# Kernel optimization log

Hardware: AMD Instinct MI355X
Metric: run time of the kernel (lower is better)

Reference implementation:

```python
import jax, jax.numpy as jnp
import numpy as np

B = 1048576
CARDS = np.array([2,2,2,2,2,3,3,4,4,4,4,4,4,5,5,5,5,5,5,5,2,2,2,2,2,2,2,2,2], dtype=np.int32)
NBR = 29  # number of categorical branches
EPS = 1e-5


def setup_inputs() -> dict:
    key = jax.random.key(0)
    ks = jax.random.split(key, 24)
    inp = {}
    inp['xcon'] = jax.random.normal(ks[0], (B, 7), dtype=jnp.float32)
    raw = jax.random.randint(ks[1], (B, NBR), 0, 5, dtype=jnp.int32)
    inp['xcat'] = raw % jnp.asarray(CARDS)[None, :]  # in-range per-branch indices
    s6 = 1.0 / np.sqrt(6.0)
    inp['emb_tables'] = jax.random.normal(ks[2], (NBR, 5, 6), dtype=jnp.float32)
    inp['w1'] = jax.random.normal(ks[3], (NBR, 6, 6), dtype=jnp.float32) * s6
    inp['b1'] = jax.random.normal(ks[4], (NBR, 6), dtype=jnp.float32) * s6
    inp['w2'] = jax.random.normal(ks[5], (NBR, 6), dtype=jnp.float32) * s6
    inp['b2'] = jax.random.normal(ks[6], (NBR,), dtype=jnp.float32) * s6
    inp['cbn_g'] = jnp.ones((7,), jnp.float32)
    inp['cbn_b'] = jnp.zeros((7,), jnp.float32)
    inp['cbn_m'] = jax.random.normal(ks[7], (7,), jnp.float32) * 0.1
    inp['cbn_v'] = jnp.ones((7,), jnp.float32) + 0.1 * jax.random.uniform(ks[8], (7,))
    dims = [(36, 36), (18, 36), (9, 18), (2, 9)]
    for i, (o, ic) in enumerate(dims, 1):
        s = 1.0 / np.sqrt(ic)
        inp[f'fc{i}_w'] = jax.random.normal(ks[8 + 2 * i], (o, ic), jnp.float32) * s
        inp[f'fc{i}_b'] = jax.random.normal(ks[9 + 2 * i], (o,), jnp.float32) * s
    for i, d in zip([1, 2, 3], [36, 18, 9]):
        inp[f'bn{i}_g'] = jnp.ones((d,), jnp.float32)
        inp[f'bn{i}_b'] = jnp.zeros((d,), jnp.float32)
        inp[f'bn{i}_m'] = jax.random.normal(jax.random.fold_in(key, 100 + i), (d,), jnp.float32) * 0.1
        inp[f'bn{i}_v'] = jnp.ones((d,), jnp.float32) + 0.1 * jax.random.uniform(jax.random.fold_in(key, 200 + i), (d,))
    return inp


def _bn(x, g, b, m, v):
    return (x - m) * jax.lax.rsqrt(v + EPS) * g + b


def reference(xcon, xcat, emb_tables, w1, b1, w2, b2,
              cbn_g, cbn_b, cbn_m, cbn_v,
              fc1_w, fc1_b, bn1_g, bn1_b, bn1_m, bn1_v,
              fc2_w, fc2_b, bn2_g, bn2_b, bn2_m, bn2_v,
              fc3_w, fc3_b, bn3_g, bn3_b, bn3_m, bn3_v,
              fc4_w, fc4_b):
    # Batched gather over all 29 branches: [B,29,6]
    emb = emb_tables[jnp.arange(NBR)[None, :], xcat]
    # Per-branch tiny MLP, fused as batched GEMMs
    h = jax.nn.relu(jnp.einsum('bjd,jde->bje', emb, w1) + b1)   # [B,29,6]
    xcatemb = jnp.einsum('bjd,jd->bj', h, w2) + b2              # [B,29]
    # (catdo_layer dropout is identity in eval mode)
    xcon_n = _bn(xcon, cbn_g, cbn_b, cbn_m, cbn_v)              # BatchNorm1d(7), eval
    xin = jnp.concatenate([xcon_n, xcatemb], axis=1)            # [B,36]
    h1 = jax.nn.relu(_bn(xin @ fc1_w.T + fc1_b, bn1_g, bn1_b, bn1_m, bn1_v))
    h2 = jax.nn.relu(_bn(h1 @ fc2_w.T + fc2_b, bn2_g, bn2_b, bn2_m, bn2_v))
    h3 = jax.nn.relu(_bn(h2 @ fc3_w.T + fc3_b, bn3_g, bn3_b, bn3_m, bn3_v))
    logits = h3 @ fc4_w.T + fc4_b                               # [B,2]
    return jax.nn.softmax(logits, axis=1)
```

## Files before the change

kernel.cpp:

```cpp
#include <hip/hip_runtime.h>

typedef _Float16 f16x8 __attribute__((ext_vector_type(8)));
typedef __fp16 fp16x2 __attribute__((ext_vector_type(2)));
typedef float f32x4 __attribute__((ext_vector_type(4)));

#define NTHR 256
constexpr float EPS = 1e-5f;
constexpr int NBLOCKS = 4096;

#define TAB_B   0
#define W1_B    1024
#define W2_B    7168
#define W3_B    11264
#define B1_B    12288
#define B2_B    12544
#define B3_B    12672
#define W4_B    12736
#define B4_B    12800

__device__ __forceinline__ ushort f16bits(float x) {
    union { _Float16 h; ushort u; } c; c.h = (_Float16)x; return c.u;
}
__device__ __forceinline__ uint pk2(float a, float b) {
    union { fp16x2 h; uint u; } c; c.h = __builtin_amdgcn_cvt_pkrtz(a, b); return c.u;
}
__device__ __forceinline__ uint pkrelu(float a, float b) {
    return pk2(fmaxf(a, 0.f), fmaxf(b, 0.f));
}
__device__ __forceinline__ f16x8 mk8(uint a, uint b, uint c, uint d) {
    union { uint u[4]; f16x8 v; } f;
    f.u[0] = a; f.u[1] = b; f.u[2] = c; f.u[3] = d;
    return f.v;
}

__device__ __forceinline__ f16x8 ldw_frag(const ushort* wp, int m, int stride, int kb, int g) {
    const ushort* p = wp + m * stride + kb + 4 * g;
    uint2 lo = *(const uint2*)p;
    uint2 hi = *(const uint2*)(p + 16);
    return mk8(lo.x, lo.y, hi.x, hi.y);
}

__global__ __launch_bounds__(NTHR) void prep_kernel(
    const float* __restrict__ embt, const float* __restrict__ w1,
    const float* __restrict__ b1,   const float* __restrict__ w2,
    const float* __restrict__ b2,
    const float* __restrict__ cbn_g, const float* __restrict__ cbn_b,
    const float* __restrict__ cbn_m, const float* __restrict__ cbn_v,
    const float* __restrict__ f1w, const float* __restrict__ f1b,
    const float* __restrict__ f2w, const float* __restrict__ f2b,
    const float* __restrict__ f3w, const float* __restrict__ f3b,
    const float* __restrict__ f4w, const float* __restrict__ f4b,
    const float* __restrict__ bn1g, const float* __restrict__ bn1b,
    const float* __restrict__ bn1m, const float* __restrict__ bn1v,
    const float* __restrict__ bn2g, const float* __restrict__ bn2b,
    const float* __restrict__ bn2m, const float* __restrict__ bn2v,
    const float* __restrict__ bn3g, const float* __restrict__ bn3b,
    const float* __restrict__ bn3m, const float* __restrict__ bn3v,
    char* __restrict__ ws)
{
    const int t = threadIdx.x;
    float* tab = (float*)(ws + TAB_B);
    ushort* w1o = (ushort*)(ws + W1_B);
    ushort* w2o = (ushort*)(ws + W2_B);
    ushort* w3o = (ushort*)(ws + W3_B);
    float* b1o = (float*)(ws + B1_B);
    float* b2o = (float*)(ws + B2_B);
    float* b3o = (float*)(ws + B3_B);
    float* w4o = (float*)(ws + W4_B);
    float* b4o = (float*)(ws + B4_B);

    for (int i = t; i < 232; i += NTHR) {
        int j = i / 8, c = i % 8;
        float xe = 0.f;
        if (c < 5) {
            xe = b2[j];
            for (int e = 0; e < 6; e++) {
                float a = b1[j * 6 + e];
                for (int d = 0; d < 6; d++)
                    a += embt[(j * 5 + c) * 6 + d] * w1[j * 36 + d * 6 + e];
                xe += fmaxf(a, 0.f) * w2[j * 6 + e];
            }
        }
        tab[i] = xe;
    }
    for (int i = t; i < 3072; i += NTHR) {
        int n = i / 64, k = i % 64;
        float v = 0.f;
        if (n < 36 && k < 36) {
            float s1 = bn1g[n] * rsqrtf(bn1v[n] + EPS);
            v = f1w[n * 36 + k] * s1;
            if (k < 7) v *= cbn_g[k] * rsqrtf(cbn_v[k] + EPS);
        }
        w1o[i] = f16bits(v);
    }
    if (t < 48) {
        float v = 0.f;
        if (t < 36) {
            float s1 = bn1g[t] * rsqrtf(bn1v[t] + EPS);
            v = f1b[t] * s1 + bn1b[t] - bn1m[t] * s1;
            for (int k = 0; k < 7; k++) {
                float cs = cbn_g[k] * rsqrtf(cbn_v[k] + EPS);
                float ct = cbn_b[k] - cbn_m[k] * cs;
                v += f1w[t * 36 + k] * s1 * ct;
            }
        }
        b1o[t] = v;
    }
    for (int i = t; i < 2048; i += NTHR) {
        int n = i / 64, k = i % 64;
        float v = 0.f;
        if (n < 18 && k < 36) {
            float s = bn2g[n] * rsqrtf(bn2v[n] + EPS);
            v = f2w[n * 36 + k] * s;
        }
        w2o[i] = f16bits(v);
    }
    if (t < 32) {
        float v = 0.f;
        if (t < 18) {
            float s = bn2g[t] * rsqrtf(bn2v[t] + EPS);
            v = f2b[t] * s + bn2b[t] - bn2m[t] * s;
        }
        b2o[t] = v;
    }
    for (int i = t; i < 512; i += NTHR) {
        int n = i / 32, k = i % 32;
        float v = 0.f;
        if (n < 9 && k < 18) {
            float s = bn3g[n] * rsqrtf(bn3v[n] + EPS);
            v = f3w[n * 18 + k] * s;
        }
        w3o[i] = f16bits(v);
    }
    if (t < 16) {
        float v = 0.f;
        if (t < 9) {
            float s = bn3g[t] * rsqrtf(bn3v[t] + EPS);
            v = f3b[t] * s + bn3b[t] - bn3m[t] * s;
        }
        b3o[t] = v;
    }
    if (t < 16) w4o[t] = (t < 9) ? (f4w[9 + t] - f4w[t]) : 0.f;
    if (t == 0) b4o[0] = f4b[1] - f4b[0];
}

#define XSTRIDE 88

__global__ __launch_bounds__(NTHR, 4) void recovery_net_kernel(
    const float* __restrict__ xcon, const int* __restrict__ xcat,
    const char* __restrict__ ws, float2* __restrict__ out)
{
    __shared__ __align__(16) char s_x[256 * XSTRIDE];
    __shared__ uint  s_catp[1856];
    __shared__ float s_xcon[1792];
    __shared__ float s_tab[464];

    const int t = threadIdx.x;
    const int lane = t & 63, w = t >> 6;
    const int l15 = lane & 15, g = lane >> 4;

    {
        const int4* src = (const int4*)(xcat + (size_t)blockIdx.x * 7424);
        for (int i = t; i < 1856; i += NTHR) {
            int4 v = src[i];
            s_catp[i] = (uint)(v.x & 0xff) | ((uint)(v.y & 0xff) << 8) |
                        ((uint)(v.z & 0xff) << 16) | ((uint)(v.w & 0xff) << 24);
        }
        const float4* s2 = (const float4*)(xcon + (size_t)blockIdx.x * 1792);
        for (int i = t; i < 448; i += NTHR) ((float4*)s_xcon)[i] = s2[i];
        const float* tws = (const float*)(ws + TAB_B);
        for (int i = t; i < 464; i += NTHR) s_tab[i] = tws[i % 232];
    }
    __syncthreads();

    {
        const unsigned char* myc = ((const unsigned char*)s_catp) + t * 29;
        const float* tb = s_tab + ((t >> 5) & 1) * 232;
        float v[36];
#pragma unroll
        for (int k = 0; k < 7; k++) v[k] = s_xcon[t * 7 + k];
#pragma unroll
        for (int j = 0; j < 29; j++) v[7 + j] = tb[j * 8 + (int)myc[j]];
        uint wd[18];
#pragma unroll
        for (int j = 0; j < 18; j++) wd[j] = pk2(v[2 * j], v[2 * j + 1]);
        char* xb = s_x + t * XSTRIDE;
#pragma unroll
        for (int j = 0; j < 9; j++)
            *(uint2*)(xb + 8 * j) = make_uint2(wd[2 * j], wd[2 * j + 1]);
    }

    const int rb = w * 64;
    const ushort* w1p = (const ushort*)(ws + W1_B);
    const ushort* w2p = (const ushort*)(ws + W2_B);
    const ushort* w3p = (const ushort*)(ws + W3_B);
    const float* b1p = (const float*)(ws + B1_B);
    const float* b2p = (const float*)(ws + B2_B);
    const float* b3p = (const float*)(ws + B3_B);
    const float* w4p = (const float*)(ws + W4_B);
    const float* b4p = (const float*)(ws + B4_B);

    f16x8 a1[3][2], a2[2][2], a3;
#pragma unroll
    for (int mt = 0; mt < 3; mt++) {
        a1[mt][0] = ldw_frag(w1p, mt * 16 + l15, 64, 0, g);
        a1[mt][1] = ldw_frag(w1p, mt * 16 + l15, 64, 32, g);
    }
#pragma unroll
    for (int mt = 0; mt < 2; mt++) {
        a2[mt][0] = ldw_frag(w2p, mt * 16 + l15, 64, 0, g);
        a2[mt][1] = ldw_frag(w2p, mt * 16 + l15, 64, 32, g);
    }
    a3 = ldw_frag(w3p, l15, 32, 0, g);

    const float4 b1v0 = *(const float4*)(b1p + 4 * g);
    const float4 b1v1 = *(const float4*)(b1p + 16 + 4 * g);
    const float4 b1v2 = *(const float4*)(b1p + 32 + 4 * g);
    const float4 b2v0 = *(const float4*)(b2p + 4 * g);
    const float4 b2v1 = *(const float4*)(b2p + 16 + 4 * g);
    const float4 b3v  = *(const float4*)(b3p + 4 * g);
    const float4 w4v  = *(const float4*)(w4p + 4 * g);
    const float b4s = *b4p;

#pragma unroll
    for (int bt = 0; bt < 4; bt++) {
        const char* xr = s_x + (rb + 16 * bt + l15) * XSTRIDE;
        uint2 q0 = *(const uint2*)(xr + 8 * g);
        uint2 q1 = *(const uint2*)(xr + 32 + 8 * g);
        uint2 q2 = *(const uint2*)(xr + 64);
        f16x8 xb0 = mk8(q0.x, q0.y, q1.x, q1.y);
        f16x8 xb1 = mk8(g == 0 ? q2.x : 0u, g == 0 ? q2.y : 0u, 0u, 0u);

        f32x4 c10 = f32x4{b1v0.x, b1v0.y, b1v0.z, b1v0.w};
        f32x4 c11 = f32x4{b1v1.x, b1v1.y, b1v1.z, b1v1.w};
        f32x4 c12 = f32x4{b1v2.x, b1v2.y, b1v2.z, b1v2.w};
        c10 = __builtin_amdgcn_mfma_f32_16x16x32_f16(a1[0][0], xb0, c10, 0, 0, 0);
        c11 = __builtin_amdgcn_mfma_f32_16x16x32_f16(a1[1][0], xb0, c11, 0, 0, 0);
        c12 = __builtin_amdgcn_mfma_f32_16x16x32_f16(a1[2][0], xb0, c12, 0, 0, 0);
        c10 = __builtin_amdgcn_mfma_f32_16x16x32_f16(a1[0][1], xb1, c10, 0, 0, 0);
        c11 = __builtin_amdgcn_mfma_f32_16x16x32_f16(a1[1][1], xb1, c11, 0, 0, 0);
        c12 = __builtin_amdgcn_mfma_f32_16x16x32_f16(a1[2][1], xb1, c12, 0, 0, 0);

        f16x8 h0 = mk8(pkrelu(c10.x, c10.y), pkrelu(c10.z, c10.w),
                       pkrelu(c11.x, c11.y), pkrelu(c11.z, c11.w));
        f16x8 h1 = mk8(pkrelu(c12.x, c12.y), pkrelu(c12.z, c12.w), 0u, 0u);

        f32x4 c20 = f32x4{b2v0.x, b2v0.y, b2v0.z, b2v0.w};
        f32x4 c21 = f32x4{b2v1.x, b2v1.y, b2v1.z, b2v1.w};
        c20 = __builtin_amdgcn_mfma_f32_16x16x32_f16(a2[0][0], h0, c20, 0, 0, 0);
        c21 = __builtin_amdgcn_mfma_f32_16x16x32_f16(a2[1][0], h0, c21, 0, 0, 0);
        c20 = __builtin_amdgcn_mfma_f32_16x16x32_f16(a2[0][1], h1, c20, 0, 0, 0);
        c21 = __builtin_amdgcn_mfma_f32_16x16x32_f16(a2[1][1], h1, c21, 0, 0, 0);

        f16x8 h2 = mk8(pkrelu(c20.x, c20.y), pkrelu(c20.z, c20.w),
                       pkrelu(c21.x, c21.y), pkrelu(c21.z, c21.w));
        f32x4 c3 = f32x4{b3v.x, b3v.y, b3v.z, b3v.w};
        c3 = __builtin_amdgcn_mfma_f32_16x16x32_f16(a3, h2, c3, 0, 0, 0);

        float part = fmaxf(c3.x, 0.f) * w4v.x + fmaxf(c3.y, 0.f) * w4v.y +
                     fmaxf(c3.z, 0.f) * w4v.z + fmaxf(c3.w, 0.f) * w4v.w;
        part += __shfl_xor(part, 16);
        part += __shfl_xor(part, 32);
        float d = part + b4s;
        float p1 = 1.f / (1.f + __expf(-d));
        if (g == 0)
            out[blockIdx.x * 256 + rb + 16 * bt + l15] = make_float2(1.f - p1, p1);
    }
}

extern "C" void kernel_launch(void* const* d_in, const int* in_sizes, int n_in,
                              void* d_out, int out_size, void* d_ws, size_t ws_size,
                              hipStream_t stream) {
    (void)in_sizes; (void)n_in; (void)ws_size; (void)out_size;
    char* ws = (char*)d_ws;
    prep_kernel<<<1, NTHR, 0, stream>>>(
        (const float*)d_in[2],  (const float*)d_in[3],
        (const float*)d_in[4],  (const float*)d_in[5],
        (const float*)d_in[6],
        (const float*)d_in[7],  (const float*)d_in[8],
        (const float*)d_in[9],  (const float*)d_in[10],
        (const float*)d_in[11], (const float*)d_in[12],
        (const float*)d_in[13], (const float*)d_in[14],
        (const float*)d_in[15], (const float*)d_in[16],
        (const float*)d_in[17], (const float*)d_in[18],
        (const float*)d_in[19], (const float*)d_in[20],
        (const float*)d_in[21], (const float*)d_in[22],
        (const float*)d_in[23], (const float*)d_in[24],
        (const float*)d_in[25], (const float*)d_in[26],
        (const float*)d_in[27], (const float*)d_in[28],
        (const float*)d_in[29], (const float*)d_in[30],
        ws);
    recovery_net_kernel<<<NBLOCKS, NTHR, 0, stream>>>(
        (const float*)d_in[0], (const int*)d_in[1], ws, (float2*)d_out);
}
```

Baseline: 77.92 us.

## Gather fp16 embedding table directly into LDS row buffer, drop staging arrays

The precomputed per-branch embedding output table is now stored as fp16. The main kernel no longer stages xcat bytes, xcon and the table in shared memory. Each thread converts its coalesced xcon and xcat vector loads straight into fp16 entries of the per-row LDS input buffer, gathering table values from global (cached) memory. Dropping the staging arrays and shrinking the row stride cuts LDS usage enough to raise launch bounds to 8 blocks per CU. The cost is scattered 2-byte LDS stores with possible bank conflicts, per-element integer divides, and global gathers from the tiny table instead of LDS reads.

```diff
diff --git a/kernel.cpp b/kernel.cpp
--- a/kernel.cpp
+++ b/kernel.cpp
@@ -59,7 +59,7 @@
     char* __restrict__ ws)
 {
     const int t = threadIdx.x;
-    float* tab = (float*)(ws + TAB_B);
+    ushort* tab = (ushort*)(ws + TAB_B);
     ushort* w1o = (ushort*)(ws + W1_B);
     ushort* w2o = (ushort*)(ws + W2_B);
     ushort* w3o = (ushort*)(ws + W3_B);
@@ -81,7 +81,7 @@
                 xe += fmaxf(a, 0.f) * w2[j * 6 + e];
             }
         }
-        tab[i] = xe;
+        tab[i] = f16bits(xe);
     }
     for (int i = t; i < 3072; i += NTHR) {
         int n = i / 64, k = i % 64;
@@ -144,51 +144,51 @@
     if (t == 0) b4o[0] = f4b[1] - f4b[0];
 }
 
-#define XSTRIDE 88
-
-__global__ __launch_bounds__(NTHR, 4) void recovery_net_kernel(
+#define XSTRIDE 72
+
+__global__ __launch_bounds__(NTHR, 8) void recovery_net_kernel(
     const float* __restrict__ xcon, const int* __restrict__ xcat,
     const char* __restrict__ ws, float2* __restrict__ out)
 {
     __shared__ __align__(16) char s_x[256 * XSTRIDE];
-    __shared__ uint  s_catp[1856];
-    __shared__ float s_xcon[1792];
-    __shared__ float s_tab[464];
 
     const int t = threadIdx.x;
     const int lane = t & 63, w = t >> 6;
     const int l15 = lane & 15, g = lane >> 4;
-
+    const ushort* tabh = (const ushort*)(ws + TAB_B);
+
+    {
+        const float4* src = (const float4*)(xcon + (size_t)blockIdx.x * 1792);
+        for (int idx = t; idx < 448; idx += NTHR) {
+            float4 v = src[idx];
+            int i0 = idx * 4;
+#pragma unroll
+            for (int e = 0; e < 4; e++) {
+                int i = i0 + e;
+                unsigned r = (unsigned)i / 7u;
+                unsigned k = (unsigned)i - r * 7u;
+                float f = (e == 0) ? v.x : (e == 1) ? v.y : (e == 2) ? v.z : v.w;
+                *(ushort*)(s_x + r * XSTRIDE + 2 * k) = f16bits(f);
+            }
+        }
+    }
     {
         const int4* src = (const int4*)(xcat + (size_t)blockIdx.x * 7424);
-        for (int i = t; i < 1856; i += NTHR) {
-            int4 v = src[i];
-            s_catp[i] = (uint)(v.x & 0xff) | ((uint)(v.y & 0xff) << 8) |
-                        ((uint)(v.z & 0xff) << 16) | ((uint)(v.w & 0xff) << 24);
-        }
-        const float4* s2 = (const float4*)(xcon + (size_t)blockIdx.x * 1792);
-        for (int i = t; i < 448; i += NTHR) ((float4*)s_xcon)[i] = s2[i];
-        const float* tws = (const float*)(ws + TAB_B);
-        for (int i = t; i < 464; i += NTHR) s_tab[i] = tws[i % 232];
+        for (int idx = t; idx < 1856; idx += NTHR) {
+            int4 v = src[idx];
+            int i0 = idx * 4;
+#pragma unroll
+            for (int e = 0; e < 4; e++) {
+                int i = i0 + e;
+                unsigned r = (unsigned)i / 29u;
+                unsigned j = (unsigned)i - r * 29u;
+                int c = (e == 0) ? v.x : (e == 1) ? v.y : (e == 2) ? v.z : v.w;
+                ushort h = tabh[j * 8 + c];
+                *(ushort*)(s_x + r * XSTRIDE + 14 + 2 * j) = h;
+            }
+        }
     }
     __syncthreads();
-
-    {
-        const unsigned char* myc = ((const unsigned char*)s_catp) + t * 29;
-        const float* tb = s_tab + ((t >> 5) & 1) * 232;
-        float v[36];
-#pragma unroll
-        for (int k = 0; k < 7; k++) v[k] = s_xcon[t * 7 + k];
-#pragma unroll
-        for (int j = 0; j < 29; j++) v[7 + j] = tb[j * 8 + (int)myc[j]];
-        uint wd[18];
-#pragma unroll
-        for (int j = 0; j < 18; j++) wd[j] = pk2(v[2 * j], v[2 * j + 1]);
-        char* xb = s_x + t * XSTRIDE;
-#pragma unroll
-        for (int j = 0; j < 9; j++)
-            *(uint2*)(xb + 8 * j) = make_uint2(wd[2 * j], wd[2 * j + 1]);
-    }
 
     const int rb = w * 64;
     const ushort* w1p = (const ushort*)(ws + W1_B);
```

Measured after the change: 143.9 us. +84.7%, slower.
